# Kernel optimization log

Measured on AMD Instinct MI355X. Metric: run time of the kernel, lower is better.

The kernel has to match this reference:

```python
import jax, jax.numpy as jnp
import numpy as np
import math

B, N, KN, CIN, COUT, NC, DIM = 4, 8192, 16, 64, 64, 16, 3


def _linear_params(key, fan_in, fan_out):
    kw, kb = jax.random.split(key)
    bound = 1.0 / math.sqrt(fan_in)
    w = jax.random.uniform(kw, (fan_in, fan_out), jnp.float32, -bound, bound)
    b = jax.random.uniform(kb, (fan_out,), jnp.float32, -bound, bound)
    return w, b


def setup_inputs() -> dict:
    key = jax.random.key(0)
    ks = jax.random.split(key, 9)
    inp = jax.random.normal(ks[0], (B, N, CIN), jnp.float32)
    points = jax.random.uniform(ks[1], (B, N, DIM), jnp.float32)
    next_pts = jax.random.uniform(ks[2], (B, N, DIM), jnp.float32)
    indices = jax.random.randint(ks[3], (B, N, KN), 0, N, jnp.int64)
    wbound = math.sqrt(3.0) * math.sqrt(2.0 / (CIN + COUT))
    weight = jax.random.uniform(ks[4], (CIN, NC, COUT), jnp.float32, -wbound, wbound)
    bias = jnp.zeros((COUT,), jnp.float32)
    # centers: points inside the unit ball (scaled uniform cube is a faithful stand-in for a learned param init)
    centers = jax.random.uniform(ks[5], (DIM, NC), jnp.float32, -1.0, 1.0) / math.sqrt(DIM)
    l1_w, l1_b = _linear_params(ks[6], DIM * NC, 2 * NC)
    l2_w, l2_b = _linear_params(ks[7], 2 * NC, NC)
    l3_w, l3_b = _linear_params(ks[8], NC, NC)
    return {
        "inp": inp, "points": points, "next_pts": next_pts, "indices": indices,
        "weight": weight, "bias": bias, "centers": centers,
        "l1_w": l1_w, "l1_b": l1_b, "l2_w": l2_w, "l2_b": l2_b,
        "l3_w": l3_w, "l3_b": l3_b, "K": KN,
    }


def reference(inp, points, next_pts, indices, weight, bias, centers,
              l1_w, l1_b, l2_w, l2_b, l3_w, l3_b, K):
    b, n, cin = inp.shape
    bidx = jnp.arange(b)[:, None, None]
    feats = inp[bidx, indices]                                # [B, N, K, Cin] gather
    pts = points[bidx, indices] - next_pts[:, :, None, :]     # [B, N, K, D] relative coords
    # distances to kernel centers -> flatten to [B, N, K, D*NC]
    d = (pts[..., :, None] - centers).reshape(b, n, K, -1)
    d = jax.nn.relu(d @ l1_w + l1_b)
    d = jax.nn.relu(d @ l2_w + l2_b)
    d = jax.nn.relu(d @ l3_w + l3_b)                          # [B, N, K, NC]
    f = jnp.einsum('bnkc,bnkm->bncm', feats, d).reshape(b, n, -1)  # [B, N, Cin*NC]
    out = (f @ weight.reshape(-1, weight.shape[-1])) / K + bias    # [B, N, Cout]
    return out
```

## Files before the change

kernel.cpp:

```cpp
#include <hip/hip_runtime.h>

#define BB    4
#define NN    8192
#define KK    16
#define CIN   64
#define COUTC 64
#define P     16

typedef short bf16x8 __attribute__((ext_vector_type(8)));
typedef float f32x4  __attribute__((ext_vector_type(4)));
typedef float f32x2  __attribute__((ext_vector_type(2)));
typedef unsigned short u16x4 __attribute__((ext_vector_type(4)));

__device__ __forceinline__ unsigned short f2bf_rne(float f) {
    unsigned int u = __builtin_bit_cast(unsigned int, f);
    u += 0x7fffu + ((u >> 16) & 1u);
    return (unsigned short)(u >> 16);
}

__device__ __forceinline__ unsigned int pack_bf2(float lo, float hi) {
    return (unsigned int)f2bf_rne(lo) | ((unsigned int)f2bf_rne(hi) << 16);
}

__global__ __launch_bounds__(256) void prep_all(
    const float* __restrict__ inp, unsigned short* __restrict__ inp_bf,
    const float* __restrict__ W, unsigned short* __restrict__ Wt,
    const float* __restrict__ l1w, const float* __restrict__ l1b,
    const float* __restrict__ centers, float* __restrict__ A1,
    const float* __restrict__ l2w, const float* __restrict__ l3w,
    unsigned short* __restrict__ Wt2, unsigned short* __restrict__ Wt3)
{
    const int blk = blockIdx.x;
    const int t   = threadIdx.x;
    if (blk < 2048) {
        const int q4 = blk * 256 + t;
        const int n  = q4 >> 4;
        const int r  = q4 & 15;
        const float* src = inp + (size_t)n * 64 + r;
        u16x4 v;
        v[0] = f2bf_rne(src[0]);
        v[1] = f2bf_rne(src[16]);
        v[2] = f2bf_rne(src[32]);
        v[3] = f2bf_rne(src[48]);
        *(u16x4*)(inp_bf + (size_t)n * 64 + r * 4) = v;
    } else if (blk < 2304) {
        const int o    = (blk - 2048) * 256 + t;
        const int cout = o >> 10;
        const int kp   = o & 1023;
        const int m    = kp >> 6;
        const int cin  = kp & 63;
        Wt[o] = f2bf_rne(W[(cin * 16 + m) * 64 + cout] * (1.0f / 16.0f));
    } else if (blk == 2304) {
        if (t < 32) {
            float bb = l1b[t];
            float a0 = 0.f, a1 = 0.f, a2 = 0.f;
            for (int c = 0; c < 16; ++c) {
                const float w0 = l1w[(c     ) * 32 + t];
                const float w1 = l1w[(16 + c) * 32 + t];
                const float w2 = l1w[(32 + c) * 32 + t];
                a0 += w0; a1 += w1; a2 += w2;
                bb -= centers[c] * w0 + centers[16 + c] * w1 + centers[32 + c] * w2;
            }
            A1[0 * 32 + t] = a0; A1[1 * 32 + t] = a1; A1[2 * 32 + t] = a2; A1[3 * 32 + t] = bb;
        }
    } else {
        for (int i = t; i < 1024; i += 256) {
            if (i < 512) {
                const int l = i >> 3, j = i & 7;
                const int k = (l >> 4) * 8 + j, col = l & 15;
                Wt2[i] = f2bf_rne(l2w[k * 16 + col]);
            } else {
                const int i3 = i - 512;
                const int l = i3 >> 3, j = i3 & 7;
                const int k = (l >> 4) * 8 + j, col = l & 15;
                Wt3[i3] = (k < 16) ? f2bf_rne(l3w[k * 16 + col]) : (unsigned short)0;
            }
        }
    }
}

__global__ __launch_bounds__(256) void ptconv_fused(
    const unsigned short* __restrict__ inp_bf,
    const float* __restrict__ points,
    const float* __restrict__ next_pts,
    const int*   __restrict__ indices,
    const unsigned short* __restrict__ Wt,
    const unsigned short* __restrict__ Wt2,
    const unsigned short* __restrict__ Wt3,
    const float* __restrict__ A1f,
    const float* __restrict__ bias,
    const float* __restrict__ l2b, const float* __restrict__ l3b,
    float* __restrict__ out)
{
    const int t    = threadIdx.x;
    const int lane = t & 63;
    const int w    = t >> 6;
    const int pt0  = blockIdx.x * P;
    const int b    = pt0 >> 13;

    __shared__ unsigned short s_u[P][512];

    char* const wb = (char*)s_u + w * 4096;
    const f32x2 zero2 = {0.f, 0.f};
    const f32x4 z4 = {0.f, 0.f, 0.f, 0.f};
    const int arow = lane & 15;
    const int hi   = lane >> 4;

    {
        const int p = t >> 4;
        const int pt = pt0 + p;
        const int id = indices[(size_t)pt0 * KK + t];
        const float* pp = points + ((size_t)(b * NN + id)) * 3;
        const float* np = next_pts + (size_t)pt * 3;
        const float px = pp[0] - np[0];
        const float py = pp[1] - np[1];
        const float pz = pp[2] - np[2];
        const f32x2 px2 = {px, px}, py2 = {py, py}, pz2 = {pz, pz};

        const f32x2* A0  = (const f32x2*)(A1f);
        const f32x2* A1v = (const f32x2*)(A1f + 32);
        const f32x2* A2  = (const f32x2*)(A1f + 64);
        const f32x2* A3  = (const f32x2*)(A1f + 96);
        unsigned int pk[16];
        #pragma unroll
        for (int j = 0; j < 16; ++j) {
            f32x2 a = __builtin_elementwise_fma(pz2, A2[j], A3[j]);
            a = __builtin_elementwise_fma(py2, A1v[j], a);
            a = __builtin_elementwise_fma(px2, A0[j], a);
            a = __builtin_elementwise_max(a, zero2);
            pk[j] = pack_bf2(a[0], a[1]);
        }
        #pragma unroll
        for (int c = 0; c < 4; ++c) {
            const unsigned int off = (unsigned)(lane * 64)
                + ((((unsigned)c) * 16u) ^ (((unsigned)(lane & 3)) << 4));
            *(uint4*)(wb + off) = make_uint4(pk[4*c], pk[4*c+1], pk[4*c+2], pk[4*c+3]);
        }
    }
    __threadfence_block();

    {
        const bf16x8 b2 = *(const bf16x8*)(Wt2 + lane * 8);
        const float bias2 = l2b[arow];
        uint2 h2sv[4];
        #pragma unroll
        for (int T = 0; T < 4; ++T) {
            const int row = T * 16 + arow;
            const unsigned int off = (unsigned)(row * 64)
                + ((((unsigned)hi) * 16u) ^ (((unsigned)(row & 3)) << 4));
            const bf16x8 a = *(const bf16x8*)(wb + off);
            const f32x4 d = __builtin_amdgcn_mfma_f32_16x16x32_bf16(a, b2, z4, 0, 0, 0);
            h2sv[T].x = pack_bf2(fmaxf(d[0] + bias2, 0.f), fmaxf(d[1] + bias2, 0.f));
            h2sv[T].y = pack_bf2(fmaxf(d[2] + bias2, 0.f), fmaxf(d[3] + bias2, 0.f));
        }
        __threadfence_block();
        #pragma unroll
        for (int T = 0; T < 4; ++T) {
            const unsigned short v0 = (unsigned short)(h2sv[T].x & 0xffffu);
            const unsigned short v1 = (unsigned short)(h2sv[T].x >> 16);
            const unsigned short v2 = (unsigned short)(h2sv[T].y & 0xffffu);
            const unsigned short v3 = (unsigned short)(h2sv[T].y >> 16);
            const int R0 = T * 16 + hi * 4;
            *(unsigned short*)(wb + ((unsigned)((R0+0) * 32 + arow * 2) ^ (((unsigned)((R0+0) & 1)) << 4))) = v0;
            *(unsigned short*)(wb + ((unsigned)((R0+1) * 32 + arow * 2) ^ (((unsigned)((R0+1) & 1)) << 4))) = v1;
            *(unsigned short*)(wb + ((unsigned)((R0+2) * 32 + arow * 2) ^ (((unsigned)((R0+2) & 1)) << 4))) = v2;
            *(unsigned short*)(wb + ((unsigned)((R0+3) * 32 + arow * 2) ^ (((unsigned)((R0+3) & 1)) << 4))) = v3;
        }
    }
    __threadfence_block();

    {
        const bf16x8 b3 = *(const bf16x8*)(Wt3 + lane * 8);
        const float bias3 = l3b[arow];
        uint2 hsave[4];
        #pragma unroll
        for (int T = 0; T < 4; ++T) {
            const int row = T * 16 + arow;
            const unsigned int off = ((unsigned)(row * 32 + hi * 16)) ^ (((unsigned)(row & 1)) << 4);
            const bf16x8 a = *(const bf16x8*)(wb + off);
            const f32x4 d = __builtin_amdgcn_mfma_f32_16x16x32_bf16(a, b3, z4, 0, 0, 0);
            hsave[T].x = pack_bf2(fmaxf(d[0] + bias3, 0.f), fmaxf(d[1] + bias3, 0.f));
            hsave[T].y = pack_bf2(fmaxf(d[2] + bias3, 0.f), fmaxf(d[3] + bias3, 0.f));
        }
        __threadfence_block();
        #pragma unroll
        for (int T = 0; T < 4; ++T) {
            const unsigned int xw = ((unsigned)(T & 3)) << 5;
            const unsigned int base = (unsigned)(T * 1024 + arow * 32 + hi * 8);
            *(uint2*)(wb + (base ^ xw)) = make_uint2(hsave[T].x, hsave[T].y);
        }
    }
    __threadfence_block();

    uint2 holdA[2][2], holdB[2][2];
    {
        const int kg   = (hi & 1) * 8;
        const unsigned short* ibase = inp_bf + (size_t)b * NN * 64;
        const int* idxg = indices + (size_t)pt0 * KK;
        const bf16x8 vzero = {0, 0, 0, 0, 0, 0, 0, 0};
        char* fbb = (char*)s_u;

        #pragma unroll
        for (int pr = 0; pr < 2; ++pr) {
            const int pA  = w * 4 + pr * 2;
            const int pB  = pA + 1;
            const int myp = (hi < 2) ? pA : pB;

            const int4 i0 = *(const int4*)&idxg[myp * 16 + kg];
            const int4 i1 = *(const int4*)&idxg[myp * 16 + kg + 4];
            const int ids[8] = {i0.x, i0.y, i0.z, i0.w, i1.x, i1.y, i1.z, i1.w};

            u16x4 rows[8];
            #pragma unroll
            for (int jj = 0; jj < 8; ++jj)
                rows[jj] = *(const u16x4*)(ibase + (size_t)ids[jj] * 64 + arow * 4);

            const unsigned int hb = ((unsigned)(myp * 1024 + arow * 32 + kg * 2))
                                    ^ (((unsigned)(myp & 3)) << 5);
            const bf16x8 vfull = *(const bf16x8*)((const char*)s_u + hb);
            const bf16x8 bfA = (hi < 2) ? vfull : vzero;
            const bf16x8 bfB = (hi < 2) ? vzero : vfull;

            #pragma unroll
            for (int tile = 0; tile < 4; ++tile) {
                bf16x8 af;
                #pragma unroll
                for (int jj = 0; jj < 8; ++jj) af[jj] = (short)rows[jj][tile];
                const f32x4 dA = __builtin_amdgcn_mfma_f32_16x16x32_bf16(af, bfA, z4, 0, 0, 0);
                const f32x4 dB = __builtin_amdgcn_mfma_f32_16x16x32_bf16(af, bfB, z4, 0, 0, 0);
                const uint2 vA = make_uint2(pack_bf2(dA[0], dA[1]), pack_bf2(dA[2], dA[3]));
                const uint2 vB = make_uint2(pack_bf2(dB[0], dB[1]), pack_bf2(dB[2], dB[3]));
                if (tile < 2) {
                    const unsigned int baseo = (unsigned)(arow * 64 + tile * 32 + hi * 8);
                    const unsigned int offA = ((unsigned)(pA * 1024) + baseo)
                                              ^ (((unsigned)((pA & 7) ^ (arow & 7))) << 4);
                    const unsigned int offB = ((unsigned)(pB * 1024) + baseo)
                                              ^ (((unsigned)((pB & 7) ^ (arow & 7))) << 4);
                    *(uint2*)(fbb + offA) = vA;
                    *(uint2*)(fbb + offB) = vB;
                } else {
                    holdA[pr][tile - 2] = vA;
                    holdB[pr][tile - 2] = vB;
                }
            }
        }
    }
    __syncthreads();

    {
        const unsigned short* wtb = Wt + (size_t)(w * 16 + arow) * 1024 + hi * 8;
        const char* fbb = (const char*)s_u;
        f32x4 acc = {0.f, 0.f, 0.f, 0.f};

        #pragma unroll
        for (int m = 0; m < 16; ++m) {
            const unsigned int xr = ((unsigned)((arow & 7) ^ (m & 7))) << 4;
            const bf16x8 av = *(const bf16x8*)(fbb +
                (((unsigned)(arow * 1024 + m * 64 + hi * 16)) ^ xr));
            const bf16x8 bv = *(const bf16x8*)(wtb + m * 64);
            acc = __builtin_amdgcn_mfma_f32_16x16x32_bf16(av, bv, acc, 0, 0, 0);
        }
        __syncthreads();

        {
            char* fbw = (char*)s_u;
            #pragma unroll
            for (int pr = 0; pr < 2; ++pr) {
                const int pA = w * 4 + pr * 2;
                const int pB = pA + 1;
                #pragma unroll
                for (int t2 = 0; t2 < 2; ++t2) {
                    const unsigned int baseo = (unsigned)(arow * 64 + t2 * 32 + hi * 8);
                    const unsigned int offA = ((unsigned)(pA * 1024) + baseo)
                                              ^ (((unsigned)((pA & 7) ^ (arow & 7))) << 4);
                    const unsigned int offB = ((unsigned)(pB * 1024) + baseo)
                                              ^ (((unsigned)((pB & 7) ^ (arow & 7))) << 4);
                    *(uint2*)(fbw + offA) = holdA[pr][t2];
                    *(uint2*)(fbw + offB) = holdB[pr][t2];
                }
            }
        }
        __syncthreads();

        #pragma unroll
        for (int m = 0; m < 16; ++m) {
            const unsigned int xr = ((unsigned)((arow & 7) ^ (m & 7))) << 4;
            const bf16x8 av = *(const bf16x8*)(fbb +
                (((unsigned)(arow * 1024 + m * 64 + hi * 16)) ^ xr));
            const bf16x8 bv = *(const bf16x8*)(wtb + m * 64 + 32);
            acc = __builtin_amdgcn_mfma_f32_16x16x32_bf16(av, bv, acc, 0, 0, 0);
        }

        const float bvs = bias[w * 16 + arow];
        #pragma unroll
        for (int r = 0; r < 4; ++r) {
            const int prow = hi * 4 + r;
            out[((size_t)(pt0 + prow)) * 64 + w * 16 + arow] = acc[r] + bvs;
        }
    }
}

extern "C" void kernel_launch(void* const* d_in, const int* in_sizes, int n_in,
                              void* d_out, int out_size, void* d_ws, size_t ws_size,
                              hipStream_t stream) {
    const float* inp      = (const float*)d_in[0];
    const float* points   = (const float*)d_in[1];
    const float* next_pts = (const float*)d_in[2];
    const int*   indices  = (const int*)  d_in[3];
    const float* weight   = (const float*)d_in[4];
    const float* bias     = (const float*)d_in[5];
    const float* centers  = (const float*)d_in[6];
    const float* l1w      = (const float*)d_in[7];
    const float* l1b      = (const float*)d_in[8];
    const float* l2w      = (const float*)d_in[9];
    const float* l2b      = (const float*)d_in[10];
    const float* l3w      = (const float*)d_in[11];
    const float* l3b      = (const float*)d_in[12];
    float* outp = (float*)d_out;

    unsigned short* Wt    = (unsigned short*)d_ws;
    float*          A1f   = (float*)((char*)d_ws + 131072);
    unsigned short* Wt2   = (unsigned short*)((char*)d_ws + 132096);
    unsigned short* Wt3   = (unsigned short*)((char*)d_ws + 133120);
    unsigned short* inpbf = (unsigned short*)((char*)d_ws + (1 << 20));

    prep_all<<<2306, 256, 0, stream>>>(inp, inpbf, weight, Wt,
                                       l1w, l1b, centers, A1f,
                                       l2w, l3w, Wt2, Wt3);

    const int grid = (BB * NN) / P;
    ptconv_fused<<<grid, 256, 0, stream>>>(inpbf, points, next_pts, indices,
                                           Wt, Wt2, Wt3, A1f, bias,
                                           l2b, l3b, outp);
}
```

Before: 52.73 us.

## Gather fp32 input directly and double shared buffer to drop resync pass

Removes the separate prep pass that converted the whole input to bf16. The fused kernel now gathers fp32 neighbour rows and converts them in registers. Shared memory per block is doubled so all four feature tiles are stored at once, which removes the register hold buffers and two __syncthreads barriers between the two accumulation halves. In exchange the gathers read twice the bytes with scalar loads, and the larger shared footprint may lower occupancy.

```diff
diff --git a/kernel.cpp b/kernel.cpp
--- a/kernel.cpp
+++ b/kernel.cpp
@@ -10,7 +10,6 @@
 typedef short bf16x8 __attribute__((ext_vector_type(8)));
 typedef float f32x4  __attribute__((ext_vector_type(4)));
 typedef float f32x2  __attribute__((ext_vector_type(2)));
-typedef unsigned short u16x4 __attribute__((ext_vector_type(4)));
 
 __device__ __forceinline__ unsigned short f2bf_rne(float f) {
     unsigned int u = __builtin_bit_cast(unsigned int, f);
@@ -23,7 +22,6 @@
 }
 
 __global__ __launch_bounds__(256) void prep_all(
-    const float* __restrict__ inp, unsigned short* __restrict__ inp_bf,
     const float* __restrict__ W, unsigned short* __restrict__ Wt,
     const float* __restrict__ l1w, const float* __restrict__ l1b,
     const float* __restrict__ centers, float* __restrict__ A1,
@@ -32,25 +30,14 @@
 {
     const int blk = blockIdx.x;
     const int t   = threadIdx.x;
-    if (blk < 2048) {
-        const int q4 = blk * 256 + t;
-        const int n  = q4 >> 4;
-        const int r  = q4 & 15;
-        const float* src = inp + (size_t)n * 64 + r;
-        u16x4 v;
-        v[0] = f2bf_rne(src[0]);
-        v[1] = f2bf_rne(src[16]);
-        v[2] = f2bf_rne(src[32]);
-        v[3] = f2bf_rne(src[48]);
-        *(u16x4*)(inp_bf + (size_t)n * 64 + r * 4) = v;
-    } else if (blk < 2304) {
-        const int o    = (blk - 2048) * 256 + t;
+    if (blk < 256) {
+        const int o    = blk * 256 + t;
         const int cout = o >> 10;
         const int kp   = o & 1023;
         const int m    = kp >> 6;
         const int cin  = kp & 63;
         Wt[o] = f2bf_rne(W[(cin * 16 + m) * 64 + cout] * (1.0f / 16.0f));
-    } else if (blk == 2304) {
+    } else if (blk == 256) {
         if (t < 32) {
             float bb = l1b[t];
             float a0 = 0.f, a1 = 0.f, a2 = 0.f;
@@ -80,7 +67,7 @@
 }
 
 __global__ __launch_bounds__(256) void ptconv_fused(
-    const unsigned short* __restrict__ inp_bf,
+    const float* __restrict__ inp,
     const float* __restrict__ points,
     const float* __restrict__ next_pts,
     const int*   __restrict__ indices,
@@ -98,9 +85,9 @@
     const int pt0  = blockIdx.x * P;
     const int b    = pt0 >> 13;
 
-    __shared__ unsigned short s_u[P][512];
-
-    char* const wb = (char*)s_u + w * 4096;
+    __shared__ unsigned short s_u[P][1024];
+
+    char* const wb = (char*)s_u + w * 8192;
     const f32x2 zero2 = {0.f, 0.f};
     const f32x4 z4 = {0.f, 0.f, 0.f, 0.f};
     const int arow = lane & 15;
@@ -186,16 +173,15 @@
         #pragma unroll
         for (int T = 0; T < 4; ++T) {
             const unsigned int xw = ((unsigned)(T & 3)) << 5;
-            const unsigned int base = (unsigned)(T * 1024 + arow * 32 + hi * 8);
+            const unsigned int base = (unsigned)(T * 2048 + arow * 32 + hi * 8);
             *(uint2*)(wb + (base ^ xw)) = make_uint2(hsave[T].x, hsave[T].y);
         }
     }
     __threadfence_block();
 
-    uint2 holdA[2][2], holdB[2][2];
-    {
-        const int kg   = (hi & 1) * 8;
-        const unsigned short* ibase = inp_bf + (size_t)b * NN * 64;
+    {
+        const int kg = (hi & 1) * 8;
+        const float* inb = inp + (size_t)b * NN * 64;
         const int* idxg = indices + (size_t)pt0 * KK;
         const bf16x8 vzero = {0, 0, 0, 0, 0, 0, 0, 0};
         char* fbb = (char*)s_u;
@@ -210,12 +196,15 @@
             const int4 i1 = *(const int4*)&idxg[myp * 16 + kg + 4];
             const int ids[8] = {i0.x, i0.y, i0.z, i0.w, i1.x, i1.y, i1.z, i1.w};
 
-            u16x4 rows[8];
+            float rf0[8], rf1[8], rf2[8], rf3[8];
             #pragma unroll
-            for (int jj = 0; jj < 8; ++jj)
-                rows[jj] = *(const u16x4*)(ibase + (size_t)ids[jj] * 64 + arow * 4);
-
-            const unsigned int hb = ((unsigned)(myp * 1024 + arow * 32 + kg * 2))
+            for (int jj = 0; jj < 8; ++jj) {
+                const float* rp = inb + (size_t)ids[jj] * 64 + arow;
+                rf0[jj] = rp[0];  rf1[jj] = rp[16];
+                rf2[jj] = rp[32]; rf3[jj] = rp[48];
+            }
+
+            const unsigned int hb = ((unsigned)(myp * 2048 + arow * 32 + kg * 2))
                                     ^ (((unsigned)(myp & 3)) << 5);
             const bf16x8 vfull = *(const bf16x8*)((const char*)s_u + hb);
             const bf16x8 bfA = (hi < 2) ? vfull : vzero;
@@ -225,23 +214,23 @@
             for (int tile = 0; tile < 4; ++tile) {
                 bf16x8 af;
                 #pragma unroll
-                for (int jj = 0; jj < 8; ++jj) af[jj] = (short)rows[jj][tile];
+                for (int jj = 0; jj < 8; ++jj) {
+                    const float v = (tile == 0) ? rf0[jj] : (tile == 1) ? rf1[jj]
+                                  : (tile == 2) ? rf2[jj] : rf3[jj];
+                    af[jj] = (short)f2bf_rne(v);
+                }
                 const f32x4 dA = __builtin_amdgcn_mfma_f32_16x16x32_bf16(af, bfA, z4, 0, 0, 0);
                 const f32x4 dB = __builtin_amdgcn_mfma_f32_16x16x32_bf16(af, bfB, z4, 0, 0, 0);
                 const uint2 vA = make_uint2(pack_bf2(dA[0], dA[1]), pack_bf2(dA[2], dA[3]));
                 const uint2 vB = make_uint2(pack_bf2(dB[0], dB[1]), pack_bf2(dB[2], dB[3]));
-                if (tile < 2) {
-                    const unsigned int baseo = (unsigned)(arow * 64 + tile * 32 + hi * 8);
-                    const unsigned int offA = ((unsigned)(pA * 1024) + baseo)
-                                              ^ (((unsigned)((pA & 7) ^ (arow & 7))) << 4);
-                    const unsigned int offB = ((unsigned)(pB * 1024) + baseo)
-                                              ^ (((unsigned)((pB & 7) ^ (arow & 7))) << 4);
-                    *(uint2*)(fbb + offA) = vA;
-                    *(uint2*)(fbb + offB) = vB;
-                } else {
-                    holdA[pr][tile - 2] = vA;
-                    holdB[pr][tile - 2] = vB;
-                }
+                const unsigned int half = (tile < 2) ? 0u : 1024u;
+                const unsigned int baseo = (unsigned)(arow * 64 + (tile & 1) * 32 + hi * 8);
+                const unsigned int offA = ((unsigned)(pA * 2048) + half + baseo)
+                                          ^ (((unsigned)((pA & 7) ^ (arow & 7))) << 4);
+                const unsigned int offB = ((unsigned)(pB * 2048) + half + baseo)
+                                          ^ (((unsigned)((pB & 7) ^ (arow & 7))) << 4);
+                *(uint2*)(fbb + offA) = vA;
+                *(uint2*)(fbb + offB) = vB;
             }
         }
     }
@@ -256,37 +245,15 @@
         for (int m = 0; m < 16; ++m) {
             const unsigned int xr = ((unsigned)((arow & 7) ^ (m & 7))) << 4;
             const bf16x8 av = *(const bf16x8*)(fbb +
-                (((unsigned)(arow * 1024 + m * 64 + hi * 16)) ^ xr));
+                (((unsigned)(arow * 2048 + m * 64 + hi * 16)) ^ xr));
             const bf16x8 bv = *(const bf16x8*)(wtb + m * 64);
             acc = __builtin_amdgcn_mfma_f32_16x16x32_bf16(av, bv, acc, 0, 0, 0);
         }
-        __syncthreads();
-
-        {
-            char* fbw = (char*)s_u;
-            #pragma unroll
-            for (int pr = 0; pr < 2; ++pr) {
-                const int pA = w * 4 + pr * 2;
-                const int pB = pA + 1;
-                #pragma unroll
-                for (int t2 = 0; t2 < 2; ++t2) {
-                    const unsigned int baseo = (unsigned)(arow * 64 + t2 * 32 + hi * 8);
-                    const unsigned int offA = ((unsigned)(pA * 1024) + baseo)
-                                              ^ (((unsigned)((pA & 7) ^ (arow & 7))) << 4);
-                    const unsigned int offB = ((unsigned)(pB * 1024) + baseo)
-                                              ^ (((unsigned)((pB & 7) ^ (arow & 7))) << 4);
-                    *(uint2*)(fbw + offA) = holdA[pr][t2];
-                    *(uint2*)(fbw + offB) = holdB[pr][t2];
-                }
-            }
-        }
-        __syncthreads();
-
         #pragma unroll
         for (int m = 0; m < 16; ++m) {
             const unsigned int xr = ((unsigned)((arow & 7) ^ (m & 7))) << 4;
             const bf16x8 av = *(const bf16x8*)(fbb +
-                (((unsigned)(arow * 1024 + m * 64 + hi * 16)) ^ xr));
+                (((unsigned)(arow * 2048 + 1024 + m * 64 + hi * 16)) ^ xr));
             const bf16x8 bv = *(const bf16x8*)(wtb + m * 64 + 32);
             acc = __builtin_amdgcn_mfma_f32_16x16x32_bf16(av, bv, acc, 0, 0, 0);
         }
@@ -322,14 +289,12 @@
     float*          A1f   = (float*)((char*)d_ws + 131072);
     unsigned short* Wt2   = (unsigned short*)((char*)d_ws + 132096);
     unsigned short* Wt3   = (unsigned short*)((char*)d_ws + 133120);
-    unsigned short* inpbf = (unsigned short*)((char*)d_ws + (1 << 20));
-
-    prep_all<<<2306, 256, 0, stream>>>(inp, inpbf, weight, Wt,
-                                       l1w, l1b, centers, A1f,
-                                       l2w, l3w, Wt2, Wt3);
+
+    prep_all<<<258, 256, 0, stream>>>(weight, Wt, l1w, l1b, centers, A1f,
+                                      l2w, l3w, Wt2, Wt3);
 
     const int grid = (BB * NN) / P;
-    ptconv_fused<<<grid, 256, 0, stream>>>(inpbf, points, next_pts, indices,
+    ptconv_fused<<<grid, 256, 0, stream>>>(inp, points, next_pts, indices,
                                            Wt, Wt2, Wt3, A1f, bias,
                                            l2b, l3b, outp);
 }
```

Result: slower. 55.88 us (+6.0%).
